# Performance work log

Measured on AMD Instinct MI355X. Metric: run time of the kernel, lower is better.

Reference implementation:

```python
import jax, jax.numpy as jnp
import numpy as np

N = 4096          # residues (2 chains x 2048)
CHAINS = 2
LMAX = 2
L = (LMAX + 1) ** 2            # 9 spherical coefficients
BBC = 32                       # bb_channels
NBB = 3                        # n_bb_atoms - 1
SPH = BBC + NBB                # 35 sphere channels fed to attention
KNN = 20
LRK = 40
HEADS = 8
HC = 32
VC = HC // 4                   # attn_value_channels = 8
EDGE_F = 32                    # 16 RBF + 16 positional
L_IDX = np.repeat(np.arange(LMAX + 1), 2 * np.arange(LMAX + 1) + 1)  # degree of each of the 9 coeffs


def so3_linear(x, w, b):
    # x: [N,L,Cin]; w: [LMAX+1,Cin,Cout] shared across m within each degree l; bias only on l=0
    out = jnp.einsum('nlc,lcd->nld', x, w[L_IDX])
    return out.at[:, 0, :].add(b)


def _rbf(d):
    mu = jnp.linspace(0.0, 20.0, 16)
    sigma = 20.0 / 16
    return jnp.exp(-(((d[..., None] - mu) / sigma) ** 2))


def _edge_pos_embed(src, dst):
    d = (src - dst).astype(jnp.float32)
    freq = jnp.exp(jnp.arange(0, 16, 2, dtype=jnp.float32) * (-np.log(10000.0) / 16))
    ang = d[:, None] * freq
    return jnp.concatenate([jnp.cos(ang), jnp.sin(ang)], axis=-1)


def setup_inputs():
    key = jax.random.key(0)
    ks = jax.random.split(key, 16)
    n = lambda i, shp, s=1.0: jax.random.normal(ks[i], shp) * s
    return {
        'X_ca': n(0, (N, 3), 10.0),
        'bb_rel': n(1, (N, NBB, 3)),
        'bb_features': n(2, (N, L, BBC)),
        'batch': jnp.repeat(jnp.arange(CHAINS), N // CHAINS),
        'x_mask': jax.random.uniform(ks[3], (N,)) < 0.02,
        'noising_mask': jax.random.uniform(ks[4], (N,)) < 0.5,
        'attn_w1': n(5, (2 * SPH + EDGE_F, HC), 0.05), 'attn_b1': jnp.zeros((HC,)),
        'attn_w2': n(6, (HC, HEADS), 0.05), 'attn_b2': jnp.zeros((HEADS,)),
        'wv': n(7, (LMAX + 1, SPH, HEADS * VC), 0.05), 'bv': jnp.zeros((HEADS * VC,)),
        'wo': n(8, (LMAX + 1, HEADS * VC, BBC), 0.05), 'bo': jnp.zeros((BBC,)),
        'wg': n(9, (BBC, BBC), 0.05), 'bg': jnp.zeros((BBC,)),
        'wf': n(10, (LMAX + 1, BBC, BBC), 0.05), 'bf': jnp.zeros((BBC,)),
        'w_xca': n(11, (LMAX + 1, BBC, 1), 0.05), 'b_xca': jnp.zeros((1,)),
        'w_gate': n(12, (BBC, 1), 0.05), 'b_gate': jnp.zeros((1,)),
        'w_bb': n(13, (LMAX + 1, BBC, NBB), 0.05), 'b_bb': jnp.zeros((NBB,)),
    }


def reference(X_ca, bb_rel, bb_features, batch, x_mask, noising_mask,
              attn_w1, attn_b1, attn_w2, attn_b2, wv, bv, wo, bo, wg, bg, wf, bf,
              w_xca, b_xca, w_gate, b_gate, w_bb, b_bb):
    Nn = X_ca.shape[0]
    BIG = jnp.float32(1e30)
    # ---- graph construction (knn_graph + sample_inv_cubic_edges) ----
    x2 = jnp.sum(X_ca * X_ca, axis=-1)
    D2 = jnp.maximum(x2[:, None] + x2[None, :] - 2.0 * (X_ca @ X_ca.T), 0.0)  # [N,N]
    same = batch[:, None] == batch[None, :]
    eye = jnp.eye(Nn, dtype=bool)
    mask_pair = x_mask[:, None] | x_mask[None, :]
    invalid = (~same) | eye | mask_pair
    knn_idx = jax.lax.top_k(-jnp.where(invalid, BIG, D2), KNN)[1]   # [N,KNN] sources per target
    # long-range: inverse-cubic distance weights, Gumbel top-k sampling, excluding knn picks
    logits = jnp.where(invalid, -BIG, -1.5 * jnp.log(D2 + 1e-6))
    rows = jnp.arange(Nn)[:, None]
    logits = logits.at[rows, knn_idx].set(-BIG)
    gumb = jax.random.gumbel(jax.random.key(1), (Nn, Nn))
    lr_idx = jax.lax.top_k(logits + gumb, LRK)[1]                   # [N,LRK]
    src = jnp.concatenate([knn_idx.reshape(-1), lr_idx.reshape(-1)])
    dst = jnp.concatenate([jnp.repeat(jnp.arange(Nn), KNN), jnp.repeat(jnp.arange(Nn), LRK)])
    # ---- edge features: RBF(dist) + relative positional embedding ----
    dvec = X_ca[src] - X_ca[dst]
    dist = jnp.linalg.norm(dvec, axis=-1)
    edge_feat = jnp.concatenate([_rbf(dist), _edge_pos_embed(src, dst)], axis=-1)  # [M,32]
    # ---- assemble SO3 node embedding [N,L,35] ----
    node = jnp.zeros((Nn, L, SPH), X_ca.dtype)
    node = node.at[:, :, :BBC].set(bb_features)
    node = node.at[:, 1:4, BBC:].set(jnp.swapaxes(bb_rel, -1, -2))  # l=1 coeffs carry bb_rel
    node = node.at[:, 0, SPH - 1].set(noising_mask.astype(X_ca.dtype))
    # ---- equivariant graph attention (simplified TransBlockV2) ----
    inv = node[:, 0, :]                                             # invariant (l=0) features
    a_in = jnp.concatenate([inv[src], inv[dst], edge_feat], axis=-1)
    h = jax.nn.silu(a_in @ attn_w1 + attn_b1)
    logit = h @ attn_w2 + attn_b2                                   # [M,HEADS]
    mx = jax.ops.segment_max(logit, dst, num_segments=Nn)
    p = jnp.exp(logit - mx[dst])
    Z = jax.ops.segment_sum(p, dst, num_segments=Nn)
    alpha = p / (Z[dst] + 1e-9)                                     # segment softmax per target/head
    v = so3_linear(node, wv, bv)[src].reshape(-1, L, HEADS, VC)     # gather source values
    msg = (v * alpha[:, None, :, None]).reshape(-1, L, HEADS * VC)
    agg = jax.ops.segment_sum(msg, dst, num_segments=Nn)            # scatter to targets
    out = so3_linear(agg, wo, bo)                                   # [N,L,32]
    gate = jax.nn.silu(out[:, 0, :] @ wg + bg)                      # invariant-gated FFN
    out = out + so3_linear(out, wf, bf) * gate[:, None, :]
    # ---- coordinate / backbone updates ----
    upd_x = so3_linear(out, w_xca, b_xca)                           # [N,L,1]
    vec = upd_x[:, 1:4, 0]                                          # l=1 -> 3-vector
    g2 = jax.nn.softplus(out[:, 0, :] @ w_gate + b_gate)            # [N,1]
    new_X = X_ca + jnp.where(noising_mask[:, None], vec * g2, 0.0)
    upd_bb = so3_linear(out, w_bb, b_bb)                            # [N,L,3]
    dbb = jnp.swapaxes(upd_bb[:, 1:4, :], -1, -2)                   # [N,3,3]
    new_bb = bb_rel + jnp.where(noising_mask[:, None, None], dbb, 0.0)
    return new_X, new_bb, out
```

## Files before the change

kernel.cpp:

```cpp
#include <hip/hip_runtime.h>
#include <hip/hip_bf16.h>
#include <stdint.h>

#define NN 4096
#define CS 2048
#define KNN 20
#define LRK 40
#define EPN 60
#define SPHC 35
#define BBCC 32
#define NHEAD 8
#define HVD 64
#define HCD 32
#define LT 9
#define MAXC 384
#define VMB ((NN*LT)/4)
#define NPB (NN/8)

#define INVAL_D2 0xFFFFFFFEu
#define CONSUMED 0xFFFFFFFFu

__device__ __forceinline__ float bflo(uint32_t d) { return __uint_as_float(d << 16); }
__device__ __forceinline__ float bfhi(uint32_t d) { return __uint_as_float(d & 0xFFFF0000u); }

__device__ __forceinline__ float fast_exp(float x) {
  return __builtin_amdgcn_exp2f(x * 1.4426950408889634f);
}
__device__ __forceinline__ float fast_cos(float a) {
  float rev = a * 0.15915494309189535f;
  rev = rev - __builtin_rintf(rev);
  return __builtin_amdgcn_cosf(rev);
}
__device__ __forceinline__ float fast_sin(float a) {
  float rev = a * 0.15915494309189535f;
  rev = rev - __builtin_rintf(rev);
  return __builtin_amdgcn_sinf(rev);
}

__device__ __forceinline__ float neglogu_f(int i, int j) {
  uint32_t c = ((uint32_t)(i & 2047) << 12) | (uint32_t)j;
  const uint32_t ks0 = 0u, ks1 = 1u, ks2 = 0x1BD11BDBu;
  uint32_t x0 = c + ks0;
  uint32_t x1 = (c + 0x800000u) + ks1;
#define TF_R(r) { x0 += x1; x1 = (x1 << (r)) | (x1 >> (32 - (r))); x1 ^= x0; }
  TF_R(13) TF_R(15) TF_R(26) TF_R(6)   x0 += ks1; x1 += ks2 + 1u;
  TF_R(17) TF_R(29) TF_R(16) TF_R(24)  x0 += ks2; x1 += ks0 + 2u;
  TF_R(13) TF_R(15) TF_R(26) TF_R(6)   x0 += ks0; x1 += ks1 + 3u;
  TF_R(17) TF_R(29) TF_R(16) TF_R(24)  x0 += ks1; x1 += ks2 + 4u;
  TF_R(13) TF_R(15) TF_R(26) TF_R(6)   x0 += ks2; x1 += ks0 + 5u;
#undef TF_R
  uint32_t b = (i >= 2048) ? x1 : x0;
  float u = __uint_as_float((b >> 9) | 0x3F800000u) - 1.0f;
  u = u + 1.17549435e-38f;
  return -0.6931471805599453f * __builtin_amdgcn_logf(u);
}

__device__ __forceinline__ void sel2l(uint32_t* val, uint32_t* hist2,
                                      uint32_t* candk, uint32_t* candp,
                                      uint32_t* sh, int* sel,
                                      int k, int base, int cb, int tid) {
  {
    uint4* h4 = (uint4*)hist2;
    uint4 z; z.x = 0; z.y = 0; z.z = 0; z.w = 0;
    h4[tid] = z; h4[tid + 256] = z;
  }
  if (tid == 0) { sh[2] = 0; sh[3] = 0; }
  __syncthreads();
  #pragma unroll
  for (int q = 0; q < 8; q++) {
    uint32_t key = val[tid + (q << 8)];
    atomicAdd(&hist2[key >> 21], 1u);
  }
  __syncthreads();
  uint32_t h[8], s = 0;
  #pragma unroll
  for (int q = 0; q < 8; q++) { h[q] = hist2[tid*8 + q]; s += h[q]; }
  uint32_t cum = s;
  #pragma unroll
  for (int off = 1; off < 64; off <<= 1) {
    uint32_t o = __shfl_up(cum, off, 64);
    if ((tid & 63) >= off) cum += o;
  }
  if ((tid & 63) == 63) sh[8 + (tid >> 6)] = cum;
  __syncthreads();
  uint32_t woff = 0;
  for (int w = 0; w < (tid >> 6); w++) woff += sh[8 + w];
  uint32_t cumAll = cum + woff;
  uint32_t cumBefore = cumAll - s;
  uint32_t rk = (uint32_t)k;
  if (rk > cumBefore && rk <= cumAll) {
    uint32_t rloc = rk - cumBefore, lp = 0;
    bool done = false;
    #pragma unroll
    for (int q = 0; q < 8; q++) {
      lp += h[q];
      if (!done && rloc <= lp) { sh[0] = (uint32_t)(tid*8 + q); sh[1] = rloc - (lp - h[q]); done = true; }
    }
  }
  __syncthreads();
  const uint32_t B = sh[0], r = sh[1];
  #pragma unroll
  for (int q = 0; q < 8; q++) {
    int pos = tid + (q << 8);
    uint32_t key = val[pos];
    if ((key >> 21) == B) {
      uint32_t idx = atomicAdd(&sh[2], 1u);
      if (idx < MAXC) { candk[idx] = key; candp[idx] = (uint32_t)pos; }
    }
  }
  __syncthreads();
  int m = (int)sh[2]; if (m > MAXC) m = MAXC;
  if (tid < 64) {
    for (int ci = tid; ci < m; ci += 64) {
      unsigned long long k64 = ((unsigned long long)candk[ci] << 32) | candp[ci];
      uint32_t rank = 0;
      for (int j = 0; j < m; j++) {
        unsigned long long o = ((unsigned long long)candk[j] << 32) | candp[j];
        rank += (o < k64) ? 1u : 0u;
      }
      if (rank == r - 1) { sh[0] = candk[ci]; sh[1] = candp[ci]; }
    }
  }
  __syncthreads();
  const uint32_t vstar = sh[0], istar = sh[1];
  #pragma unroll
  for (int q = 0; q < 8; q++) {
    int pos = tid + (q << 8);
    uint32_t key = val[pos];
    if (key < vstar || (key == vstar && (uint32_t)pos <= istar)) {
      uint32_t slot = atomicAdd(&sh[3], 1u);
      sel[base + (int)slot] = cb + pos;
    }
  }
  __syncthreads();
}

__global__ __launch_bounds__(256) void graph_kernel(const float* __restrict__ X,
                                                    const int* __restrict__ batch,
                                                    const int* __restrict__ xmask,
                                                    const int* __restrict__ nmask,
                                                    const float* __restrict__ bbf,
                                                    const float* __restrict__ bbrel,
                                                    const float* __restrict__ wv,
                                                    const float* __restrict__ bv,
                                                    const float* __restrict__ w1,
                                                    const float* __restrict__ b1,
                                                    int* __restrict__ srcO,
                                                    __hip_bfloat16* __restrict__ V,
                                                    float* __restrict__ Pn,
                                                    float* __restrict__ Pd) {
#pragma clang fp contract(off)
  const int tid = threadIdx.x;
  if (blockIdx.x >= NN + VMB) {
    int t = tid & 31;
    int n = (blockIdx.x - NN - VMB) * 8 + (tid >> 5);
    float bv_ = bbf[(size_t)n * (LT*BBCC) + t];
    float an = 0.f, ad = b1[t];
    #pragma unroll 8
    for (int c = 0; c < BBCC; c++) {
      float bc = __shfl(bv_, (tid & 32) + c, 64);
      an = fmaf(bc, w1[c * HCD + t], an);
      ad = fmaf(bc, w1[(SPHC + c) * HCD + t], ad);
    }
    float nm = nmask[n] ? 1.f : 0.f;
    an = fmaf(nm, w1[34 * HCD + t], an);
    ad = fmaf(nm, w1[69 * HCD + t], ad);
    Pn[n * HCD + t] = an;
    Pd[n * HCD + t] = ad;
    return;
  }
  if (blockIdx.x >= NN) {
    int row = (blockIdx.x - NN) * 4 + (tid >> 6);
    int d = tid & 63;
    int n = row / LT, l = row % LT;
    int li = (l == 0) ? 0 : (l < 4 ? 1 : 2);
    const float* w = wv + (size_t)li * SPHC * HVD;
    float acc = (l == 0) ? bv[d] : 0.f;
    const float* nb = bbf + (size_t)(n*LT + l) * BBCC;
    for (int c = 0; c < BBCC; c++) acc = fmaf(nb[c], w[c*HVD + d], acc);
    if (l >= 1 && l < 4) {
      for (int b = 0; b < 3; b++)
        acc = fmaf(bbrel[(size_t)(n*3 + b)*3 + (l-1)], w[(32+b)*HVD + d], acc);
    }
    if (l == 0) acc = fmaf(nmask[n] ? 1.f : 0.f, w[34*HVD + d], acc);
    V[(size_t)row * HVD + d] = __float2bfloat16(acc);
    return;
  }
  __shared__ uint32_t val[CS];
  __shared__ uint32_t hist2[2048];
  __shared__ uint32_t candk[MAXC];
  __shared__ uint32_t candp[MAXC];
  __shared__ uint32_t sh[12];
  __shared__ int sel[EPN];
  const int i = blockIdx.x;

  if (xmask[i]) {
    if (tid < KNN) srcO[(size_t)i * EPN + tid] = tid;
    else if (tid < EPN) srcO[(size_t)i * EPN + tid] = tid - KNN;
    return;
  }
  const int cb = batch[i] * CS;
  const float xi0 = X[i*3+0], xi1 = X[i*3+1], xi2 = X[i*3+2];
  const float x2i = (xi0*xi0 + xi1*xi1) + xi2*xi2;

  #pragma unroll
  for (int q = 0; q < 8; q++) {
    int pos = tid + (q << 8);
    int j = cb + pos;
    float xj0 = X[j*3+0], xj1 = X[j*3+1], xj2 = X[j*3+2];
    float x2j = (xj0*xj0 + xj1*xj1) + xj2*xj2;
    bool inval = (xmask[j] != 0) || (j == i);
    float dot = xi0*xj0 + xi1*xj1 + xi2*xj2;
    float d2r = (x2i + x2j) - 2.0f*dot;
    float d2 = d2r > 0.0f ? d2r : 0.0f;
    val[pos] = inval ? INVAL_D2 : __float_as_uint(d2);
  }
  __syncthreads();

  sel2l(val, hist2, candk, candp, sh, sel, KNN, 0, cb, tid);

  if (tid < KNN) val[sel[tid] - cb] = CONSUMED;
  __syncthreads();

  #pragma unroll
  for (int q = 0; q < 8; q++) {
    int pos = tid + (q << 8);
    uint32_t v = val[pos];
    uint32_t skey;
    if (v >= INVAL_D2) skey = CONSUMED;
    else {
      float d2p = __uint_as_float(v) + 1e-6f;
      float w = d2p * sqrtf(d2p) * neglogu_f(i, cb + pos);
      skey = __float_as_uint(w);
    }
    val[pos] = skey;
  }
  __syncthreads();

  sel2l(val, hist2, candk, candp, sh, sel, LRK, KNN, cb, tid);

  if (tid < EPN) srcO[(size_t)i * EPN + tid] = sel[tid];
}

__global__ __launch_bounds__(256) void edge_kernel(const int* __restrict__ src,
                                                   const float* __restrict__ X,
                                                   const float* __restrict__ Pn,
                                                   const float* __restrict__ Pd,
                                                   const float* __restrict__ w1,
                                                   const float* __restrict__ w2,
                                                   const float* __restrict__ b2,
                                                   float* __restrict__ logitO) {
  const float FR[8] = {1.0f, 0.31622776601683794f, 0.1f, 0.031622776601683794f,
                       0.01f, 0.0031622776601683794f, 0.001f, 0.00031622776601683794f};
  __shared__ float w1cf[BBCC][HCD];
  __shared__ float w2f[HCD][NHEAD];
  __shared__ float b2f[NHEAD];
  __shared__ float ef[8][BBCC];
  __shared__ float hbuf[8][HCD];
  int tid = threadIdx.x;
  for (int q = tid; q < BBCC*HCD; q += 256) w1cf[q >> 5][q & 31] = w1[70*HCD + q];
  if (tid < HCD*NHEAD) w2f[tid >> 3][tid & 7] = w2[tid];
  if (tid < NHEAD) b2f[tid] = b2[tid];
  int sub = tid >> 5, t = tid & 31;
  int e = blockIdx.x * 8 + sub;
  int d = e / EPN;
  int s = src[e];
  float dx = X[s*3+0] - X[d*3+0];
  float dy = X[s*3+1] - X[d*3+1];
  float dz = X[s*3+2] - X[d*3+2];
  float dist = sqrtf(dx*dx + dy*dy + dz*dz);
  if (t < 16) {
    float mu = (20.0f / 15.0f) * (float)t;
    float zz = (dist - mu) / 1.25f;
    ef[sub][t] = fast_exp(-zz * zz);
  } else {
    int k = t - 16;
    float del = (float)(s - d);
    float a = del * FR[k & 7];
    ef[sub][t] = (k < 8) ? fast_cos(a) : fast_sin(a);
  }
  __syncthreads();
  float a = Pn[s * HCD + t] + Pd[d * HCD + t];
  #pragma unroll
  for (int k = 0; k < BBCC; k++) a = fmaf(ef[sub][k], w1cf[k][t], a);
  hbuf[sub][t] = a / (1.f + fast_exp(-a));
  __syncthreads();
  if (tid < 64) {
    int e2 = tid >> 3, hh = tid & 7;
    float lg = b2f[hh];
    #pragma unroll
    for (int c = 0; c < HCD; c++) lg = fmaf(hbuf[e2][c], w2f[c][hh], lg);
    logitO[(size_t)(blockIdx.x * 8 + e2) * NHEAD + hh] = lg;
  }
}

__global__ __launch_bounds__(64) void node_kernel(const int* __restrict__ src,
                                                  const float* __restrict__ logit,
                                                  const __hip_bfloat16* __restrict__ V,
                                                  const float* __restrict__ wo,
                                                  const float* __restrict__ bo,
                                                  const float* __restrict__ wg,
                                                  const float* __restrict__ bg,
                                                  const float* __restrict__ wf,
                                                  const float* __restrict__ bfb,
                                                  const float* __restrict__ w_xca,
                                                  const float* __restrict__ w_gate,
                                                  const float* __restrict__ b_gate,
                                                  const float* __restrict__ w_bb,
                                                  const float* __restrict__ X,
                                                  const float* __restrict__ bbrel,
                                                  const int* __restrict__ nmask,
                                                  float* __restrict__ out) {
  const int n = blockIdx.x, t = threadIdx.x;
  __shared__ float alpha[EPN][NHEAD];
  __shared__ int slist[EPN];
  __shared__ float agg[LT][HVD];
  __shared__ float o0[LT][BBCC];
  __shared__ float ofin[LT][BBCC];
  __shared__ float gate[BBCC];
  if (t < EPN) slist[t] = src[(size_t)n * EPN + t];
  for (int q = t; q < EPN * NHEAD; q += 64) alpha[q >> 3][q & 7] = logit[(size_t)n * 480 + q];
  __syncthreads();
  if (t < NHEAD) {
    float m = -1e30f;
    for (int e = 0; e < EPN; e++) m = fmaxf(m, alpha[e][t]);
    float Z = 0.f;
    for (int e = 0; e < EPN; e++) { float p = expf(alpha[e][t] - m); alpha[e][t] = p; Z += p; }
    float iz = 1.f / (Z + 1e-9f);
    for (int e = 0; e < EPN; e++) alpha[e][t] *= iz;
  }
  __syncthreads();
  {
    const int h = (t & 31) >> 2;
    const bool tail = (t < 32);
    float a0 = 0.f, a1 = 0.f, a2 = 0.f, a3 = 0.f, a4 = 0.f;
    float b0 = 0.f, b1_ = 0.f, b2_ = 0.f, b3 = 0.f, b4 = 0.f;
    for (int e = 0; e < EPN; e++) {
      const uint32_t* Vr = (const uint32_t*)(V + (size_t)slist[e] * (LT * HVD));
      uint32_t d0 = Vr[t];
      uint32_t d1 = Vr[t + 64];
      uint32_t d2 = Vr[t + 128];
      uint32_t d3 = Vr[t + 192];
      uint32_t d4 = tail ? Vr[t + 256] : 0u;
      float a = alpha[e][h];
      a0 = fmaf(a, bflo(d0), a0);  b0  = fmaf(a, bfhi(d0), b0);
      a1 = fmaf(a, bflo(d1), a1);  b1_ = fmaf(a, bfhi(d1), b1_);
      a2 = fmaf(a, bflo(d2), a2);  b2_ = fmaf(a, bfhi(d2), b2_);
      a3 = fmaf(a, bflo(d3), a3);  b3  = fmaf(a, bfhi(d3), b3);
      a4 = fmaf(a, bflo(d4), a4);  b4  = fmaf(a, bfhi(d4), b4);
    }
    const int l0 = t >> 5, c = 2 * (t & 31);
    agg[l0 + 0][c] = a0;  agg[l0 + 0][c + 1] = b0;
    agg[l0 + 2][c] = a1;  agg[l0 + 2][c + 1] = b1_;
    agg[l0 + 4][c] = a2;  agg[l0 + 4][c + 1] = b2_;
    agg[l0 + 6][c] = a3;  agg[l0 + 6][c + 1] = b3;
    if (tail) { agg[8][c] = a4;  agg[8][c + 1] = b4; }
  }
  __syncthreads();
  for (int idx = t; idx < LT * BBCC; idx += 64) {
    int l = idx >> 5, d = idx & 31;
    int li = (l == 0) ? 0 : (l < 4 ? 1 : 2);
    float a = (l == 0) ? bo[d] : 0.f;
    const float* w = wo + (size_t)li * HVD * BBCC;
    for (int c = 0; c < HVD; c++) a = fmaf(agg[l][c], w[c * BBCC + d], a);
    o0[l][d] = a;
  }
  __syncthreads();
  if (t < BBCC) {
    float a = bg[t];
    for (int c = 0; c < BBCC; c++) a = fmaf(o0[0][c], wg[c * BBCC + t], a);
    gate[t] = a / (1.f + expf(-a));
  }
  __syncthreads();
  for (int idx = t; idx < LT * BBCC; idx += 64) {
    int l = idx >> 5, d = idx & 31;
    int li = (l == 0) ? 0 : (l < 4 ? 1 : 2);
    float a = (l == 0) ? bfb[d] : 0.f;
    const float* w = wf + (size_t)li * BBCC * BBCC;
    for (int c = 0; c < BBCC; c++) a = fmaf(o0[l][c], w[c * BBCC + d], a);
    float r = o0[l][d] + a * gate[d];
    ofin[l][d] = r;
    out[49152 + (size_t)n * 288 + idx] = r;
  }
  __syncthreads();
  if (t < 16) {
    float a2 = b_gate[0];
    for (int c = 0; c < BBCC; c++) a2 = fmaf(ofin[0][c], w_gate[c], a2);
    float g2 = fmaxf(a2, 0.f) + log1pf(expf(-fabsf(a2)));
    bool noise = nmask[n] != 0;
    if (t < 3) {
      float a = 0.f;
      for (int d2 = 0; d2 < BBCC; d2++) a = fmaf(ofin[1 + t][d2], w_xca[32 + d2], a);
      float nx = X[n * 3 + t] + (noise ? a * g2 : 0.f);
      out[(size_t)n * 3 + t] = nx;
    }
    if (t < 9) {
      int b = t / 3, c = t % 3;
      float a = 0.f;
      for (int d2 = 0; d2 < BBCC; d2++) a = fmaf(ofin[1 + c][d2], w_bb[(32 + d2) * 3 + b], a);
      float nb = bbrel[(size_t)(n * 3 + b) * 3 + c] + (noise ? a : 0.f);
      out[12288 + (size_t)n * 9 + b * 3 + c] = nb;
    }
  }
}

extern "C" void kernel_launch(void* const* d_in, const int* in_sizes, int n_in,
                              void* d_out, int out_size, void* d_ws, size_t ws_size,
                              hipStream_t stream) {
  (void)in_sizes; (void)n_in; (void)out_size;
  const float* X      = (const float*)d_in[0];
  const float* bbrel  = (const float*)d_in[1];
  const float* bbf    = (const float*)d_in[2];
  const int* batch    = (const int*)d_in[3];
  const int* xmask    = (const int*)d_in[4];
  const int* nmask    = (const int*)d_in[5];
  const float* w1     = (const float*)d_in[6];
  const float* b1     = (const float*)d_in[7];
  const float* w2     = (const float*)d_in[8];
  const float* b2     = (const float*)d_in[9];
  const float* wv     = (const float*)d_in[10];
  const float* bv     = (const float*)d_in[11];
  const float* wo     = (const float*)d_in[12];
  const float* bo     = (const float*)d_in[13];
  const float* wg     = (const float*)d_in[14];
  const float* bg     = (const float*)d_in[15];
  const float* wf     = (const float*)d_in[16];
  const float* bfb    = (const float*)d_in[17];
  const float* w_xca  = (const float*)d_in[18];
  const float* w_gate = (const float*)d_in[20];
  const float* b_gate = (const float*)d_in[21];
  const float* w_bb   = (const float*)d_in[22];

  if (ws_size < 18939904) return;
  char* ws = (char*)d_ws;
  int*      srcl  = (int*)(ws + 0);
  float*    logit = (float*)(ws + 983040);
  __hip_bfloat16* V = (__hip_bfloat16*)(ws + 8847360);
  float*    Pn    = (float*)(ws + 13565952);
  float*    Pd    = (float*)(ws + 14090240);
  float*    out   = (float*)d_out;

  graph_kernel<<<NN + VMB + NPB, 256, 0, stream>>>(X, batch, xmask, nmask, bbf, bbrel,
                                                   wv, bv, w1, b1, srcl, V, Pn, Pd);
  edge_kernel<<<(NN * EPN) / 8, 256, 0, stream>>>(srcl, X, Pn, Pd, w1, w2, b2, logit);
  node_kernel<<<NN, 64, 0, stream>>>(srcl, logit, V, wo, bo, wg, bg, wf, bfb,
                                     w_xca, w_gate, b_gate, w_bb, X, bbrel, nmask, out);
}
```

Before: 248.4 us.

## Fuse kNN and long-range key/histogram builds and shrink radix-select passes

The graph kernel now computes the distance keys and the sampled long-range weight keys in one pass, building both 1024-bin histograms with atomics during key generation. This removes the separate histogram passes and the second sweep over all candidates. The kNN picks are subtracted from the weight histogram. The select routine now emits elements from lower buckets directly and scans only the boundary-bucket candidates for the final inclusion pass, instead of rescanning all 2048 keys. It also adds a 4x unroll on the edge-aggregation loop. The costs are extra shared memory (two value arrays and two histograms) and coarser buckets, which could overflow the candidate buffer more often.

```diff
diff --git a/kernel.cpp b/kernel.cpp
--- a/kernel.cpp
+++ b/kernel.cpp
@@ -55,47 +55,34 @@
   return -0.6931471805599453f * __builtin_amdgcn_logf(u);
 }
 
-__device__ __forceinline__ void sel2l(uint32_t* val, uint32_t* hist2,
-                                      uint32_t* candk, uint32_t* candp,
-                                      uint32_t* sh, int* sel,
-                                      int k, int base, int cb, int tid) {
-  {
-    uint4* h4 = (uint4*)hist2;
-    uint4 z; z.x = 0; z.y = 0; z.z = 0; z.w = 0;
-    h4[tid] = z; h4[tid + 256] = z;
-  }
+__device__ __forceinline__ void pick(const uint32_t* val, const uint32_t* hist,
+                                     uint32_t* candk, uint32_t* candp,
+                                     uint32_t* sh, int* sel,
+                                     int k, int base, int cb, int tid) {
   if (tid == 0) { sh[2] = 0; sh[3] = 0; }
-  __syncthreads();
-  #pragma unroll
-  for (int q = 0; q < 8; q++) {
-    uint32_t key = val[tid + (q << 8)];
-    atomicAdd(&hist2[key >> 21], 1u);
-  }
-  __syncthreads();
-  uint32_t h[8], s = 0;
-  #pragma unroll
-  for (int q = 0; q < 8; q++) { h[q] = hist2[tid*8 + q]; s += h[q]; }
+  uint32_t h0 = hist[4*tid], h1 = hist[4*tid+1], h2 = hist[4*tid+2], h3 = hist[4*tid+3];
+  uint32_t s = h0 + h1 + h2 + h3;
   uint32_t cum = s;
   #pragma unroll
   for (int off = 1; off < 64; off <<= 1) {
     uint32_t o = __shfl_up(cum, off, 64);
     if ((tid & 63) >= off) cum += o;
   }
-  if ((tid & 63) == 63) sh[8 + (tid >> 6)] = cum;
+  if ((tid & 63) == 63) sh[4 + (tid >> 6)] = cum;
   __syncthreads();
   uint32_t woff = 0;
-  for (int w = 0; w < (tid >> 6); w++) woff += sh[8 + w];
+  for (int w = 0; w < (tid >> 6); w++) woff += sh[4 + w];
   uint32_t cumAll = cum + woff;
   uint32_t cumBefore = cumAll - s;
   uint32_t rk = (uint32_t)k;
   if (rk > cumBefore && rk <= cumAll) {
-    uint32_t rloc = rk - cumBefore, lp = 0;
-    bool done = false;
-    #pragma unroll
-    for (int q = 0; q < 8; q++) {
-      lp += h[q];
-      if (!done && rloc <= lp) { sh[0] = (uint32_t)(tid*8 + q); sh[1] = rloc - (lp - h[q]); done = true; }
-    }
+    uint32_t r0 = rk - cumBefore, d, sub;
+    if (r0 <= h0)            { d = 0; sub = 0; }
+    else if (r0 <= h0+h1)    { d = 1; sub = h0; }
+    else if (r0 <= h0+h1+h2) { d = 2; sub = h0 + h1; }
+    else                     { d = 3; sub = h0 + h1 + h2; }
+    sh[0] = 4u*tid + d;
+    sh[1] = r0 - sub;
   }
   __syncthreads();
   const uint32_t B = sh[0], r = sh[1];
@@ -103,13 +90,17 @@
   for (int q = 0; q < 8; q++) {
     int pos = tid + (q << 8);
     uint32_t key = val[pos];
-    if ((key >> 21) == B) {
-      uint32_t idx = atomicAdd(&sh[2], 1u);
+    uint32_t b = key >> 22;
+    if (b < B) {
+      uint32_t slot = atomicAdd(&sh[2], 1u);
+      sel[base + (int)slot] = cb + pos;
+    } else if (b == B) {
+      uint32_t idx = atomicAdd(&sh[3], 1u);
       if (idx < MAXC) { candk[idx] = key; candp[idx] = (uint32_t)pos; }
     }
   }
   __syncthreads();
-  int m = (int)sh[2]; if (m > MAXC) m = MAXC;
+  int m = (int)sh[3]; if (m > MAXC) m = MAXC;
   if (tid < 64) {
     for (int ci = tid; ci < m; ci += 64) {
       unsigned long long k64 = ((unsigned long long)candk[ci] << 32) | candp[ci];
@@ -123,13 +114,13 @@
   }
   __syncthreads();
   const uint32_t vstar = sh[0], istar = sh[1];
-  #pragma unroll
-  for (int q = 0; q < 8; q++) {
-    int pos = tid + (q << 8);
-    uint32_t key = val[pos];
-    if (key < vstar || (key == vstar && (uint32_t)pos <= istar)) {
-      uint32_t slot = atomicAdd(&sh[3], 1u);
-      sel[base + (int)slot] = cb + pos;
+  if (tid < 64) {
+    for (int ci = tid; ci < m; ci += 64) {
+      uint32_t ck = candk[ci], cp = candp[ci];
+      if (ck < vstar || (ck == vstar && cp <= istar)) {
+        uint32_t slot = atomicAdd(&sh[2], 1u);
+        sel[base + (int)slot] = cb + (int)cp;
+      }
     }
   }
   __syncthreads();
@@ -186,11 +177,13 @@
     V[(size_t)row * HVD + d] = __float2bfloat16(acc);
     return;
   }
-  __shared__ uint32_t val[CS];
-  __shared__ uint32_t hist2[2048];
+  __shared__ uint32_t valD[CS];
+  __shared__ uint32_t valW[CS];
+  __shared__ uint32_t histD[1024];
+  __shared__ uint32_t histW[1024];
   __shared__ uint32_t candk[MAXC];
   __shared__ uint32_t candp[MAXC];
-  __shared__ uint32_t sh[12];
+  __shared__ uint32_t sh[8];
   __shared__ int sel[EPN];
   const int i = blockIdx.x;
 
@@ -202,6 +195,13 @@
   const int cb = batch[i] * CS;
   const float xi0 = X[i*3+0], xi1 = X[i*3+1], xi2 = X[i*3+2];
   const float x2i = (xi0*xi0 + xi1*xi1) + xi2*xi2;
+
+  {
+    uint4* hD = (uint4*)histD; uint4* hW = (uint4*)histW;
+    uint4 z; z.x = 0; z.y = 0; z.z = 0; z.w = 0;
+    hD[tid] = z; hW[tid] = z;
+  }
+  __syncthreads();
 
   #pragma unroll
   for (int q = 0; q < 8; q++) {
@@ -213,31 +213,33 @@
     float dot = xi0*xj0 + xi1*xj1 + xi2*xj2;
     float d2r = (x2i + x2j) - 2.0f*dot;
     float d2 = d2r > 0.0f ? d2r : 0.0f;
-    val[pos] = inval ? INVAL_D2 : __float_as_uint(d2);
-  }
-  __syncthreads();
-
-  sel2l(val, hist2, candk, candp, sh, sel, KNN, 0, cb, tid);
-
-  if (tid < KNN) val[sel[tid] - cb] = CONSUMED;
-  __syncthreads();
-
-  #pragma unroll
-  for (int q = 0; q < 8; q++) {
-    int pos = tid + (q << 8);
-    uint32_t v = val[pos];
-    uint32_t skey;
-    if (v >= INVAL_D2) skey = CONSUMED;
-    else {
-      float d2p = __uint_as_float(v) + 1e-6f;
-      float w = d2p * sqrtf(d2p) * neglogu_f(i, cb + pos);
-      skey = __float_as_uint(w);
-    }
-    val[pos] = skey;
-  }
-  __syncthreads();
-
-  sel2l(val, hist2, candk, candp, sh, sel, LRK, KNN, cb, tid);
+    if (inval) {
+      valD[pos] = INVAL_D2;
+      valW[pos] = CONSUMED;
+    } else {
+      uint32_t kd = __float_as_uint(d2);
+      valD[pos] = kd;
+      atomicAdd(&histD[kd >> 22], 1u);
+      float d2p = d2 + 1e-6f;
+      float w = d2p * sqrtf(d2p) * neglogu_f(i, j);
+      uint32_t kw = __float_as_uint(w);
+      valW[pos] = kw;
+      atomicAdd(&histW[kw >> 22], 1u);
+    }
+  }
+  __syncthreads();
+
+  pick(valD, histD, candk, candp, sh, sel, KNN, 0, cb, tid);
+
+  if (tid < KNN) {
+    int pos = sel[tid] - cb;
+    uint32_t kw = valW[pos];
+    atomicSub(&histW[kw >> 22], 1u);
+    valW[pos] = CONSUMED;
+  }
+  __syncthreads();
+
+  pick(valW, histW, candk, candp, sh, sel, LRK, KNN, cb, tid);
 
   if (tid < EPN) srcO[(size_t)i * EPN + tid] = sel[tid];
 }
@@ -335,6 +337,7 @@
     const bool tail = (t < 32);
     float a0 = 0.f, a1 = 0.f, a2 = 0.f, a3 = 0.f, a4 = 0.f;
     float b0 = 0.f, b1_ = 0.f, b2_ = 0.f, b3 = 0.f, b4 = 0.f;
+    #pragma unroll 4
     for (int e = 0; e < EPN; e++) {
       const uint32_t* Vr = (const uint32_t*)(V + (size_t)slist[e] * (LT * HVD));
       uint32_t d0 = Vr[t];
```

New measurement: 248.6 us. Within noise of the previous version (+0.1%).
